# Performance work log

Hardware: AMD Instinct MI355X
Metric: run time of the kernel (lower is better)

Reference implementation:

```python
import jax, jax.numpy as jnp
import numpy as np

D_IN, H1, H2, N_CLS, BATCH = 1024, 2048, 2048, 1000, 8192


def setup_inputs() -> dict:
    key = jax.random.key(0)
    ks = jax.random.split(key, 7)
    x = jax.random.normal(ks[0], (BATCH, D_IN), dtype=jnp.float32)
    # torch.nn.Linear default init scale ~ 1/sqrt(fan_in); weights stored [out, in]
    W1 = jax.random.normal(ks[1], (H1, D_IN), dtype=jnp.float32) / np.sqrt(D_IN).astype(np.float32)
    b1 = jax.random.normal(ks[2], (H1,), dtype=jnp.float32) * 0.01
    W2 = jax.random.normal(ks[3], (H2, H1), dtype=jnp.float32) / np.sqrt(H1).astype(np.float32)
    b2 = jax.random.normal(ks[4], (H2,), dtype=jnp.float32) * 0.01
    W3 = jax.random.normal(ks[5], (N_CLS, H2), dtype=jnp.float32) / np.sqrt(H2).astype(np.float32)
    b3 = jax.random.normal(ks[6], (N_CLS,), dtype=jnp.float32) * 0.01
    return {"x": x, "W1": W1, "b1": b1, "W2": W2, "b2": b2, "W3": W3, "b3": b3}


def reference(x, W1, b1, W2, b2, W3, b3):
    # forward_with_coactivations: classifier = [Linear, ReLU, Linear, ReLU, Linear]
    # activation points: the two ReLU layers and the final Linear.
    prev_act = (x > 0).astype(jnp.float32)  # [B, D_IN]

    z1 = x @ W1.T + b1                      # [B, H1]
    a1 = jax.nn.relu(z1)
    act1 = (z1 > 0).astype(jnp.float32)     # (relu(z)>0) == (z>0)
    # sum_s outer(prev_act[s], act1[s]) == prev_act.T @ act1
    coact0 = jnp.einsum('bi,bj->ij', prev_act, act1)  # [D_IN, H1]

    z2 = a1 @ W2.T + b2                     # [B, H2]
    a2 = jax.nn.relu(z2)
    act2 = (z2 > 0).astype(jnp.float32)
    coact1 = jnp.einsum('bi,bj->ij', act1, act2)      # [H1, H2]

    logits = a2 @ W3.T + b3                 # [B, N_CLS]
    act3 = (logits > 0).astype(jnp.float32)
    coact2 = jnp.einsum('bi,bj->ij', act2, act3)      # [H2, N_CLS]

    return logits, coact0, coact1, coact2
```

## Files before the change

kernel.cpp:

```cpp
#include <hip/hip_runtime.h>
#include <hip/hip_bf16.h>


typedef short v8s __attribute__((ext_vector_type(8)));
typedef float v4f __attribute__((ext_vector_type(4)));
typedef int v4i __attribute__((ext_vector_type(4)));

enum { MODE_RELU = 0, MODE_LOGITS = 1 };

__device__ __forceinline__ void async_cp16(const void* gsrc, void* ldst) {
  __builtin_amdgcn_global_load_lds(
      (const __attribute__((address_space(1))) void*)gsrc,
      (__attribute__((address_space(3))) void*)ldst, 16, 0, 0);
}

#define FENCE asm volatile("" ::: "memory")
#define BAR()                         \
  do {                                \
    FENCE;                            \
    __builtin_amdgcn_s_barrier();     \
    FENCE;                            \
  } while (0)
#define WAITL()                                          \
  do {                                                   \
    asm volatile("s_waitcnt lgkmcnt(0)" ::: "memory");   \
    __builtin_amdgcn_sched_barrier(0);                   \
  } while (0)
#define WAITV(n)                                           \
  do {                                                     \
    asm volatile("s_waitcnt vmcnt(" #n ")" ::: "memory");  \
    __builtin_amdgcn_sched_barrier(0);                     \
  } while (0)
#define PRIO1 __builtin_amdgcn_s_setprio(1)
#define PRIO0 __builtin_amdgcn_s_setprio(0)

__global__ __launch_bounds__(512, 2) void gemm256_relu_wt(
    const __hip_bfloat16* __restrict__ A, const __hip_bfloat16* __restrict__ B,
    const float* __restrict__ bias, __hip_bfloat16* __restrict__ Cout,
    char* __restrict__ Tout, int K, int ldc) {
  __shared__ char smem[131072];
  const int t = threadIdx.x;
  const int m0 = blockIdx.y * 256;
  const int n0 = blockIdx.x * 256;

  const int c0 = t, c1 = 512 + t;
  const int r0s = c0 >> 3, r1s = c1 >> 3;
  const int goff0 = r0s * K + ((c0 & 7) ^ (r0s & 7)) * 8;
  const int goff1 = r1s * K + ((c1 & 7) ^ (r1s & 7)) * 8;
  const int loff0 = c0 * 16, loff1 = c1 * 16;

  const __hip_bfloat16* const Abase = A + (size_t)m0 * K;
  const __hip_bfloat16* const Bbase = B + (size_t)n0 * K;
  const size_t hk = (size_t)128 * K;

  char* const pA0l = smem;
  char* const pA0h = smem + 16384;
  char* const pB0l = smem + 32768;
  char* const pB0h = smem + 49152;
  char* const pA1l = smem + 65536;
  char* const pA1h = smem + 81920;
  char* const pB1l = smem + 98304;
  char* const pB1h = smem + 114688;

  const int lane = t & 63;
  const int wave = t >> 6;
  const int wm = wave >> 2;
  const int wn = wave & 3;
  const int lrow = lane & 15;
  const int quad = lane >> 4;
  const int sl0 = ((quad ^ (lrow & 7)) * 16);
  const int sl1 = (((quad + 4) ^ (lrow & 7)) * 16);
  const int ardA = (wm * 128 + lrow) * 128;
  const int ardB = (wn * 64 + lrow) * 128;

  v4f acc[8][4] = {};
  v8s alo[4][2], ahi[4][2], blo[2][2], bhi[2][2];

#define STAGE(dst, src)                                               \
  do {                                                                \
    async_cp16((const void*)((src) + goff0), (void*)((dst) + loff0)); \
    async_cp16((const void*)((src) + goff1), (void*)((dst) + loff1)); \
  } while (0)

#define LDA_H(dst, hh, bb)                                                   \
  _Pragma("unroll") for (int mi = 0; mi < 4; mi++) {                         \
    dst[mi][0] =                                                             \
        *(const v8s*)(smem + (bb) + ardA + (hh)*8192 + mi * 2048 + sl0);     \
    dst[mi][1] =                                                             \
        *(const v8s*)(smem + (bb) + ardA + (hh)*8192 + mi * 2048 + sl1);     \
  }

#define LDB_P(dst, pp, bb)                                                    \
  _Pragma("unroll") for (int ni = 0; ni < 2; ni++) {                          \
    dst[ni][0] = *(const v8s*)(smem + (bb) + 32768 + ardB +                   \
                               ((pp)*2 + ni) * 2048 + sl0);                   \
    dst[ni][1] = *(const v8s*)(smem + (bb) + 32768 + ardB +                   \
                               ((pp)*2 + ni) * 2048 + sl1);                   \
  }

#define MMA_Q(af, bf, MB, NB)                                               \
  _Pragma("unroll") for (int mi = 0; mi < 4; mi++)                          \
      _Pragma("unroll") for (int ni = 0; ni < 2; ni++)                      \
          _Pragma("unroll") for (int ks = 0; ks < 2; ks++)                  \
              acc[(MB) + mi][(NB) + ni] =                                   \
      __builtin_amdgcn_mfma_f32_16x16x32_bf16(                              \
          af[mi][ks], bf[ni][ks], acc[(MB) + mi][(NB) + ni], 0, 0, 0);

  STAGE(pA0l, Abase);
  STAGE(pA0h, Abase + hk);
  STAGE(pB0l, Bbase);
  STAGE(pB0h, Bbase + hk);
  STAGE(pA1l, Abase + 64);
  WAITV(8);
  BAR();

  const int NI = K >> 7;
  const int NT = K >> 6;

#pragma unroll 1
  for (int i = 0; i < NI; ++i) {
    const int to = 2 * i + 1;
    const int t2 = (2 * i + 2 < NT) ? 2 * i + 2 : 0;
    const int t3 = (2 * i + 3 < NT) ? 2 * i + 3 : 0;
    const __hip_bfloat16* Ao = Abase + to * 64;
    const __hip_bfloat16* Bo = Bbase + to * 64;
    const __hip_bfloat16* A2 = Abase + t2 * 64;
    const __hip_bfloat16* B2 = Bbase + t2 * 64;
    const __hip_bfloat16* A3 = Abase + t3 * 64;
    LDA_H(alo, 0, 0);
    STAGE(pA1h, Ao + hk);
    WAITV(6);
    BAR();
    WAITL();
    if (i) { PRIO1; MMA_Q(ahi, bhi, 4, 2); PRIO0; }
    BAR();
    LDB_P(blo, 0, 0);
    STAGE(pB1l, Bo);
    WAITV(10);
    BAR();
    WAITL();
    PRIO1; MMA_Q(alo, blo, 0, 0); PRIO0;
    BAR();
    LDA_H(ahi, 1, 0);
    STAGE(pB1h, Bo + hk);
    WAITV(8);
    BAR();
    WAITL();
    PRIO1; MMA_Q(ahi, blo, 4, 0); PRIO0;
    BAR();
    LDB_P(bhi, 1, 0);
    STAGE(pA0l, A2);
    WAITV(8);
    BAR();
    WAITL();
    PRIO1; MMA_Q(alo, bhi, 0, 2); PRIO0;
    BAR();
    LDA_H(alo, 0, 65536);
    STAGE(pA0h, A2 + hk);
    WAITV(6);
    BAR();
    WAITL();
    PRIO1; MMA_Q(ahi, bhi, 4, 2); PRIO0;
    BAR();
    LDB_P(blo, 0, 65536);
    STAGE(pB0l, B2);
    WAITV(10);
    BAR();
    WAITL();
    PRIO1; MMA_Q(alo, blo, 0, 0); PRIO0;
    BAR();
    LDA_H(ahi, 1, 65536);
    STAGE(pB0h, B2 + hk);
    WAITV(8);
    BAR();
    WAITL();
    PRIO1; MMA_Q(ahi, blo, 4, 0); PRIO0;
    BAR();
    LDB_P(bhi, 1, 65536);
    STAGE(pA1l, A3);
    WAITV(8);
    BAR();
    WAITL();
    PRIO1; MMA_Q(alo, bhi, 0, 2); PRIO0;
    BAR();
  }
  PRIO1; MMA_Q(ahi, bhi, 4, 2); PRIO0;
  WAITV(0);
  BAR();
#undef STAGE
#undef LDA_H
#undef LDB_P
#undef MMA_Q

  float bv[4];
#pragma unroll
  for (int ni = 0; ni < 4; ni++) bv[ni] = bias[n0 + wn * 64 + ni * 16 + lrow];

#pragma unroll
  for (int mi = 0; mi < 8; mi++) {
    const int rowb = m0 + wm * 128 + mi * 16 + quad * 4;
#pragma unroll
    for (int ni = 0; ni < 4; ni++) {
      const int col = n0 + wn * 64 + ni * 16 + lrow;
#pragma unroll
      for (int r = 0; r < 4; r++) {
        const float v = acc[mi][ni][r] + bv[ni];
        Cout[(size_t)(rowb + r) * ldc + col] =
            __float2bfloat16(v > 0.f ? v : 0.f);
      }
    }
  }

  char* const sT = smem;
#pragma unroll
  for (int ni = 0; ni < 4; ni++) {
    const int c = wn * 64 + ni * 16 + lrow;
#pragma unroll
    for (int mi = 0; mi < 8; mi++) {
      const int rw = wm * 128 + mi * 16 + quad * 4;
      char4 bits;
      bits.x = (acc[mi][ni][0] + bv[ni] > 0.f) ? 1 : 0;
      bits.y = (acc[mi][ni][1] + bv[ni] > 0.f) ? 1 : 0;
      bits.z = (acc[mi][ni][2] + bv[ni] > 0.f) ? 1 : 0;
      bits.w = (acc[mi][ni][3] + bv[ni] > 0.f) ? 1 : 0;
      *(char4*)&sT[c * 272 + rw] = bits;
    }
  }
  __syncthreads();
  const int rw2 = t >> 1;
  const int hf = (t & 1) * 128;
  char* dst = Tout + (size_t)(n0 + rw2) * 8192 + m0 + hf;
  const char* src = sT + rw2 * 272 + hf;
#pragma unroll
  for (int j = 0; j < 8; j++)
    *(int4*)(dst + j * 16) = *(const int4*)(src + j * 16);
}

template <int MODE, int WT>
__global__ __launch_bounds__(256) void gemm_nt(
    const __hip_bfloat16* __restrict__ A, const __hip_bfloat16* __restrict__ B,
    const float* __restrict__ bias, void* __restrict__ Cout,
    char* __restrict__ Tout, int M, int N, int K, int n_store, int ldc) {
  __shared__ char smem[32768];
  __hip_bfloat16* sA = (__hip_bfloat16*)smem;
  __hip_bfloat16* sB = (__hip_bfloat16*)(smem + 16384);
  const int t = threadIdx.x;
  const int m0 = blockIdx.y * 128;
  const int n0 = blockIdx.x * 128;

  const __hip_bfloat16* aG[4];
  const __hip_bfloat16* bG[4];
  char* lA[4];
  char* lB[4];
#pragma unroll
  for (int j = 0; j < 4; j++) {
    const int c = j * 256 + t;
    const int row = c >> 3;
    const int g = (c & 7) ^ (row & 7);
    aG[j] = A + (size_t)(m0 + row) * K + g * 8;
    bG[j] = B + (size_t)(n0 + row) * K + g * 8;
    lA[j] = (char*)sA + c * 16;
    lB[j] = (char*)sB + c * 16;
  }

  const int lane = t & 63;
  const int wave = t >> 6;
  const int wm = (wave & 1) * 64;
  const int wn = (wave >> 1) * 64;
  const int lrow = lane & 15;
  const int quad = lane >> 4;

  const int g0 = quad ^ (lrow & 7);
  const __hip_bfloat16* pa0 = sA + (wm + lrow) * 64 + g0 * 8;
  const __hip_bfloat16* pa1 = sA + (wm + lrow) * 64 + (g0 ^ 4) * 8;
  const __hip_bfloat16* pb0 = sB + (wn + lrow) * 64 + g0 * 8;
  const __hip_bfloat16* pb1 = sB + (wn + lrow) * 64 + (g0 ^ 4) * 8;

  v4f acc[4][4] = {};

  for (int k0 = 0; k0 < K; k0 += 64) {
#pragma unroll
    for (int j = 0; j < 4; j++) {
      async_cp16(aG[j] + k0, lA[j]);
      async_cp16(bG[j] + k0, lB[j]);
    }
    __syncthreads();

    v8s a0[4], b0[4], a1[4], b1[4];
#pragma unroll
    for (int i = 0; i < 4; i++) {
      a0[i] = *(const v8s*)(pa0 + i * 16 * 64);
      b0[i] = *(const v8s*)(pb0 + i * 16 * 64);
    }
#pragma unroll
    for (int mi = 0; mi < 4; mi++)
#pragma unroll
      for (int ni = 0; ni < 4; ni++)
        acc[mi][ni] = __builtin_amdgcn_mfma_f32_16x16x32_bf16(
            a0[mi], b0[ni], acc[mi][ni], 0, 0, 0);
#pragma unroll
    for (int i = 0; i < 4; i++) {
      a1[i] = *(const v8s*)(pa1 + i * 16 * 64);
      b1[i] = *(const v8s*)(pb1 + i * 16 * 64);
    }
#pragma unroll
    for (int mi = 0; mi < 4; mi++)
#pragma unroll
      for (int ni = 0; ni < 4; ni++)
        acc[mi][ni] = __builtin_amdgcn_mfma_f32_16x16x32_bf16(
            a1[mi], b1[ni], acc[mi][ni], 0, 0, 0);
    __syncthreads();
  }

  float bvv[4];
#pragma unroll
  for (int ni = 0; ni < 4; ni++) {
    const int col = n0 + wn + ni * 16 + lrow;
    bvv[ni] = 0.f;
    if (MODE == MODE_RELU) bvv[ni] = bias[col];
    else if (col < n_store) bvv[ni] = bias[col];
  }

#pragma unroll
  for (int ni = 0; ni < 4; ni++) {
    const int col = n0 + wn + ni * 16 + lrow;
#pragma unroll
    for (int mi = 0; mi < 4; mi++) {
      const int rowb = m0 + wm + mi * 16 + quad * 4;
#pragma unroll
      for (int r = 0; r < 4; r++) {
        const int row = rowb + r;
        const float v = acc[mi][ni][r] + bvv[ni];
        if (MODE == MODE_RELU) {
          ((__hip_bfloat16*)Cout)[(size_t)row * ldc + col] =
              __float2bfloat16(v > 0.f ? v : 0.f);
        } else {
          if (col < n_store)
            ((float*)Cout)[(size_t)row * ldc + col] = v;
        }
      }
    }
  }

  if (WT) {
    char* sT = smem;
#pragma unroll
    for (int ni = 0; ni < 4; ni++) {
      const int c = wn + ni * 16 + lrow;
#pragma unroll
      for (int mi = 0; mi < 4; mi++) {
        const int r = wm + mi * 16 + quad * 4;
        char4 bits;
        bits.x = (acc[mi][ni][0] + bvv[ni] > 0.f) ? 1 : 0;
        bits.y = (acc[mi][ni][1] + bvv[ni] > 0.f) ? 1 : 0;
        bits.z = (acc[mi][ni][2] + bvv[ni] > 0.f) ? 1 : 0;
        bits.w = (acc[mi][ni][3] + bvv[ni] > 0.f) ? 1 : 0;
        *(char4*)&sT[c * 144 + r] = bits;
      }
    }
    __syncthreads();
    const int c2 = t >> 1;
    const int hf = (t & 1) * 64;
    char* dst = Tout + (size_t)(n0 + c2) * 8192 + m0 + hf;
    const char* src = sT + c2 * 144 + hf;
#pragma unroll
    for (int j = 0; j < 4; j++)
      *(int4*)(dst + j * 16) = *(const int4*)(src + j * 16);
  }
}

__global__ __launch_bounds__(256) void gemm_nt_i8(
    const char* __restrict__ A, const char* __restrict__ B,
    float* __restrict__ P, int M, int N, int Kc, int n_store, size_t slice) {
  __shared__ char sA[128 * 128];
  __shared__ char sB[128 * 128];
  const int t = threadIdx.x;
  const int m0 = blockIdx.y * 128;
  const int n0 = blockIdx.x * 128;
  const int kbeg = blockIdx.z * Kc;
  const int kend = kbeg + Kc;
  const size_t K = (size_t)Kc * gridDim.z;
  float* __restrict__ Pz = P + (size_t)blockIdx.z * slice;

  const char* aG[4];
  const char* bG[4];
  char* lA[4];
  char* lB[4];
#pragma unroll
  for (int j = 0; j < 4; j++) {
    const int c = j * 256 + t;
    const int row = c >> 3;
    const int g = (c & 7) ^ (row & 7);
    aG[j] = A + (size_t)(m0 + row) * K + g * 16;
    bG[j] = B + (size_t)(n0 + row) * K + g * 16;
    lA[j] = sA + c * 16;
    lB[j] = sB + c * 16;
  }

  const int lane = t & 63;
  const int wave = t >> 6;
  const int wm = (wave & 1) * 64;
  const int wn = (wave >> 1) * 64;
  const int lrow = lane & 15;
  const int quad = lane >> 4;

  const int g0 = quad ^ (lrow & 7);
  const char* pa0 = sA + (wm + lrow) * 128 + g0 * 16;
  const char* pa1 = sA + (wm + lrow) * 128 + (g0 ^ 4) * 16;
  const char* pb0 = sB + (wn + lrow) * 128 + g0 * 16;
  const char* pb1 = sB + (wn + lrow) * 128 + (g0 ^ 4) * 16;

  v4i acc[4][4] = {};

  for (int k0 = kbeg; k0 < kend; k0 += 128) {
#pragma unroll
    for (int j = 0; j < 4; j++) {
      async_cp16(aG[j] + k0, lA[j]);
      async_cp16(bG[j] + k0, lB[j]);
    }
    __syncthreads();

    v4i a0[4], b0[4], a1[4], b1[4];
#pragma unroll
    for (int i = 0; i < 4; i++) {
      a0[i] = *(const v4i*)(pa0 + i * 16 * 128);
      b0[i] = *(const v4i*)(pb0 + i * 16 * 128);
    }
#pragma unroll
    for (int mi = 0; mi < 4; mi++)
#pragma unroll
      for (int ni = 0; ni < 4; ni++)
        acc[mi][ni] = __builtin_amdgcn_mfma_i32_16x16x64_i8(
            a0[mi], b0[ni], acc[mi][ni], 0, 0, 0);
#pragma unroll
    for (int i = 0; i < 4; i++) {
      a1[i] = *(const v4i*)(pa1 + i * 16 * 128);
      b1[i] = *(const v4i*)(pb1 + i * 16 * 128);
    }
#pragma unroll
    for (int mi = 0; mi < 4; mi++)
#pragma unroll
      for (int ni = 0; ni < 4; ni++)
        acc[mi][ni] = __builtin_amdgcn_mfma_i32_16x16x64_i8(
            a1[mi], b1[ni], acc[mi][ni], 0, 0, 0);
    __syncthreads();
  }

#pragma unroll
  for (int ni = 0; ni < 4; ni++) {
    const int col = n0 + wn + ni * 16 + lrow;
    if (col >= n_store) continue;
#pragma unroll
    for (int mi = 0; mi < 4; mi++) {
      const int rowb = m0 + wm + mi * 16 + quad * 4;
#pragma unroll
      for (int r = 0; r < 4; r++) {
        Pz[(size_t)(rowb + r) * n_store + col] = (float)acc[mi][ni][r];
      }
    }
  }
}

template <int Z>
__global__ __launch_bounds__(256) void reduce_part(
    const float* __restrict__ P, float* __restrict__ out, int n4, size_t slice) {
  const int i = blockIdx.x * 256 + threadIdx.x;
  if (i >= n4) return;
  float4 s = ((const float4*)P)[i];
#pragma unroll
  for (int z = 1; z < Z; z++) {
    const float4 v = ((const float4*)(P + (size_t)z * slice))[i];
    s.x += v.x; s.y += v.y; s.z += v.z; s.w += v.w;
  }
  ((float4*)out)[i] = s;
}

__global__ __launch_bounds__(256) void transpose_bin8f(
    const float* __restrict__ in, char* __restrict__ out,
    int R, int ldin, int Cphys) {
  __shared__ char tile[64][65];
  const int c0 = blockIdx.x * 64;
  const int r0 = blockIdx.y * 64;
  const int tx = threadIdx.x & 63;
  const int ty = threadIdx.x >> 6;
#pragma unroll
  for (int i = 0; i < 64; i += 4) {
    const int c = c0 + tx;
    const int r = r0 + ty + i;
    float v = 0.f;
    if (c < Cphys) v = in[(size_t)r * ldin + c];
    tile[ty + i][tx] = (v > 0.f) ? 1 : 0;
  }
  __syncthreads();
  const int u = threadIdx.x & 15;
  const int cg = threadIdx.x >> 4;
#pragma unroll
  for (int i = 0; i < 64; i += 16) {
    const int col = cg + i;
    char4 v;
    v.x = tile[4 * u + 0][col];
    v.y = tile[4 * u + 1][col];
    v.z = tile[4 * u + 2][col];
    v.w = tile[4 * u + 3][col];
    *(char4*)&out[(size_t)(c0 + col) * R + r0 + 4 * u] = v;
  }
}

struct Cvt4 {
  const float* src[4];
  __hip_bfloat16* dst[4];
  int n4[4];
};
__global__ __launch_bounds__(256) void f32_to_bf16_multi(Cvt4 c) {
  int i = blockIdx.x * 256 + threadIdx.x;
#pragma unroll
  for (int s = 0; s < 4; s++) {
    if (i < c.n4[s]) {
      const float4 v = ((const float4*)c.src[s])[i];
      union { __hip_bfloat16 h[4]; ushort4 u; } cv;
      cv.h[0] = __float2bfloat16(v.x);
      cv.h[1] = __float2bfloat16(v.y);
      cv.h[2] = __float2bfloat16(v.z);
      cv.h[3] = __float2bfloat16(v.w);
      ((ushort4*)c.dst[s])[i] = cv.u;
      return;
    }
    i -= c.n4[s];
  }
}

extern "C" void kernel_launch(void* const* d_in, const int* in_sizes, int n_in,
                              void* d_out, int out_size, void* d_ws, size_t ws_size,
                              hipStream_t stream) {
  const float* x  = (const float*)d_in[0];
  const float* W1 = (const float*)d_in[1];
  const float* b1 = (const float*)d_in[2];
  const float* W2 = (const float*)d_in[3];
  const float* b2 = (const float*)d_in[4];
  const float* W3 = (const float*)d_in[5];
  const float* b3 = (const float*)d_in[6];

  float* logits = (float*)d_out;
  float* coact0 = logits + (size_t)8192 * 1000;
  float* coact1 = coact0 + (size_t)1024 * 2048;
  float* coact2 = coact1 + (size_t)2048 * 2048;

  char* ws = (char*)d_ws;
  size_t off = 0;
  auto alloc = [&](size_t bytes) {
    char* p = ws + off;
    off += (bytes + 255) & ~(size_t)255;
    return p;
  };
  __hip_bfloat16* X   = (__hip_bfloat16*)alloc((size_t)8192 * 1024 * 2);
  __hip_bfloat16* W1b = (__hip_bfloat16*)alloc((size_t)2048 * 1024 * 2);
  __hip_bfloat16* W2b = (__hip_bfloat16*)alloc((size_t)2048 * 2048 * 2);
  __hip_bfloat16* W3b = (__hip_bfloat16*)alloc((size_t)1024 * 2048 * 2);
  __hip_bfloat16* A1  = (__hip_bfloat16*)alloc((size_t)8192 * 2048 * 2);
  __hip_bfloat16* A2  = (__hip_bfloat16*)alloc((size_t)8192 * 2048 * 2);
  char* T0 = (char*)alloc((size_t)1024 * 8192);
  char* T1 = (char*)alloc((size_t)2048 * 8192);
  char* T2 = (char*)X;
  char* T3 = (char*)W2b;
  float* P = (float*)A1;

  const dim3 blk(256);

  {
    Cvt4 c;
    c.src[0] = x;  c.dst[0] = X;   c.n4[0] = 8192 * 1024 / 4;
    c.src[1] = W1; c.dst[1] = W1b; c.n4[1] = 2048 * 1024 / 4;
    c.src[2] = W2; c.dst[2] = W2b; c.n4[2] = 2048 * 2048 / 4;
    c.src[3] = W3; c.dst[3] = W3b; c.n4[3] = 1000 * 2048 / 4;
    const int total = c.n4[0] + c.n4[1] + c.n4[2] + c.n4[3];
    f32_to_bf16_multi<<<(total + 255) / 256, blk, 0, stream>>>(c);
  }

  transpose_bin8f<<<dim3(16, 128), blk, 0, stream>>>(x, T0, 8192, 1024, 1024);

  gemm256_relu_wt<<<dim3(8, 32), dim3(512), 0, stream>>>(
      X, W1b, b1, A1, T1, 1024, 2048);

  gemm256_relu_wt<<<dim3(8, 32), dim3(512), 0, stream>>>(
      A1, W2b, b2, A2, T2, 2048, 2048);

  gemm_nt<MODE_LOGITS, 1><<<dim3(8, 64), blk, 0, stream>>>(
      A2, W3b, b3, logits, T3, 8192, 1024, 2048, 1000, 1000);

  gemm_nt_i8<<<dim3(16, 8, 4), blk, 0, stream>>>(T0, T1, P,
                                                 1024, 2048, 2048, 2048,
                                                 (size_t)1024 * 2048);
  reduce_part<4><<<1024 * 2048 / 4 / 256, blk, 0, stream>>>(
      P, coact0, 1024 * 2048 / 4, (size_t)1024 * 2048);

  gemm_nt_i8<<<dim3(16, 16, 2), blk, 0, stream>>>(T1, T2, P,
                                                  2048, 2048, 4096, 2048,
                                                  (size_t)2048 * 2048);
  reduce_part<2><<<2048 * 2048 / 4 / 256, blk, 0, stream>>>(
      P, coact1, 2048 * 2048 / 4, (size_t)2048 * 2048);

  gemm_nt_i8<<<dim3(8, 16, 4), blk, 0, stream>>>(T2, T3, P,
                                                 2048, 1024, 2048, 1000,
                                                 (size_t)2048 * 1000);
  reduce_part<4><<<2048 * 1000 / 4 / 256, blk, 0, stream>>>(
      P, coact2, 2048 * 1000 / 4, (size_t)2048 * 1000);
}
```

Baseline: 421.4 us.

## Software-pipeline LDS fragment loads with MFMA using partial lgkmcnt waits

Restructures the main GEMM loop so each MFMA quarter runs on fragments loaded in the previous phase while the next fragment loads are still in flight. Partial lgkmcnt waits replace full waits, and the A-low fragment is double-buffered (aloA/aloB). Half of the workgroup barriers per iteration are removed. This hides LDS read latency behind matrix math, at the cost of extra registers that may pressure occupancy at 2 blocks per CU, and relies on exact lgkmcnt counts being correct.

```diff
diff --git a/kernel.cpp b/kernel.cpp
--- a/kernel.cpp
+++ b/kernel.cpp
@@ -26,6 +26,11 @@
     asm volatile("s_waitcnt lgkmcnt(0)" ::: "memory");   \
     __builtin_amdgcn_sched_barrier(0);                   \
   } while (0)
+#define WAITLN(n)                                           \
+  do {                                                      \
+    asm volatile("s_waitcnt lgkmcnt(" #n ")" ::: "memory"); \
+    __builtin_amdgcn_sched_barrier(0);                      \
+  } while (0)
 #define WAITV(n)                                           \
   do {                                                     \
     asm volatile("s_waitcnt vmcnt(" #n ")" ::: "memory");  \
@@ -74,7 +79,7 @@
   const int ardB = (wn * 64 + lrow) * 128;
 
   v4f acc[8][4] = {};
-  v8s alo[4][2], ahi[4][2], blo[2][2], bhi[2][2];
+  v8s aloA[4][2], aloB[4][2], ahi[4][2], blo[2][2], bhi[2][2];
 
 #define STAGE(dst, src)                                               \
   do {                                                                \
@@ -127,63 +132,57 @@
     const __hip_bfloat16* A2 = Abase + t2 * 64;
     const __hip_bfloat16* B2 = Bbase + t2 * 64;
     const __hip_bfloat16* A3 = Abase + t3 * 64;
-    LDA_H(alo, 0, 0);
+    LDA_H(aloA, 0, 0);
     STAGE(pA1h, Ao + hk);
+    WAITLN(8);
+    if (i) { PRIO1; MMA_Q(aloB, bhi, 0, 2); PRIO0; }
     WAITV(6);
-    BAR();
-    WAITL();
-    if (i) { PRIO1; MMA_Q(ahi, bhi, 4, 2); PRIO0; }
     BAR();
     LDB_P(blo, 0, 0);
     STAGE(pB1l, Bo);
+    WAITLN(4);
+    if (i) { PRIO1; MMA_Q(ahi, bhi, 4, 2); PRIO0; }
     WAITV(10);
-    BAR();
-    WAITL();
-    PRIO1; MMA_Q(alo, blo, 0, 0); PRIO0;
     BAR();
     LDA_H(ahi, 1, 0);
     STAGE(pB1h, Bo + hk);
+    WAITLN(8);
+    PRIO1; MMA_Q(aloA, blo, 0, 0); PRIO0;
     WAITV(8);
-    BAR();
-    WAITL();
-    PRIO1; MMA_Q(ahi, blo, 4, 0); PRIO0;
     BAR();
     LDB_P(bhi, 1, 0);
     STAGE(pA0l, A2);
+    WAITLN(4);
+    PRIO1; MMA_Q(ahi, blo, 4, 0); PRIO0;
     WAITV(8);
     BAR();
-    WAITL();
-    PRIO1; MMA_Q(alo, bhi, 0, 2); PRIO0;
-    BAR();
-    LDA_H(alo, 0, 65536);
+    LDA_H(aloB, 0, 65536);
     STAGE(pA0h, A2 + hk);
+    WAITLN(8);
+    PRIO1; MMA_Q(aloA, bhi, 0, 2); PRIO0;
     WAITV(6);
-    BAR();
-    WAITL();
-    PRIO1; MMA_Q(ahi, bhi, 4, 2); PRIO0;
     BAR();
     LDB_P(blo, 0, 65536);
     STAGE(pB0l, B2);
+    WAITLN(4);
+    PRIO1; MMA_Q(ahi, bhi, 4, 2); PRIO0;
     WAITV(10);
-    BAR();
-    WAITL();
-    PRIO1; MMA_Q(alo, blo, 0, 0); PRIO0;
     BAR();
     LDA_H(ahi, 1, 65536);
     STAGE(pB0h, B2 + hk);
+    WAITLN(8);
+    PRIO1; MMA_Q(aloB, blo, 0, 0); PRIO0;
     WAITV(8);
-    BAR();
-    WAITL();
-    PRIO1; MMA_Q(ahi, blo, 4, 0); PRIO0;
     BAR();
     LDB_P(bhi, 1, 65536);
     STAGE(pA1l, A3);
+    WAITLN(4);
+    PRIO1; MMA_Q(ahi, blo, 4, 0); PRIO0;
     WAITV(8);
     BAR();
-    WAITL();
-    PRIO1; MMA_Q(alo, bhi, 0, 2); PRIO0;
-    BAR();
-  }
+  }
+  WAITL();
+  PRIO1; MMA_Q(aloB, bhi, 0, 2); PRIO0;
   PRIO1; MMA_Q(ahi, bhi, 4, 2); PRIO0;
   WAITV(0);
   BAR();
```

New measurement: 456.0 us. 1.08x slower.
